# Performance work log

Hardware: AMD Instinct MI355X
Metric: run time of the kernel (lower is better)

## Reference

```python
import jax, jax.numpy as jnp
import numpy as np

B, N, C, DP, H, P = 1, 768, 384, 128, 12, 4
HP3 = H * P * 3


def setup_inputs() -> dict:
    key = jax.random.key(0)
    ks = jax.random.split(key, 16)
    w = lambda k, shp: (jax.random.normal(k, shp, jnp.float32) * 0.02)
    inp = {
        'single': jax.random.normal(ks[0], (B, N, C), jnp.float32),
        'pair': jax.random.normal(ks[1], (B, N, N, DP), jnp.float32),
        'rot': jax.random.normal(ks[2], (B, N, 3, 3), jnp.float32),
        'trans': jax.random.normal(ks[3], (B, N, 3), jnp.float32),
        'q_w': w(ks[4], (C, C)), 'q_b': jnp.zeros((C,), jnp.float32),
        'k_w': w(ks[5], (C, C)), 'k_b': jnp.zeros((C,), jnp.float32),
        'v_w': w(ks[6], (C, C)), 'v_b': jnp.zeros((C,), jnp.float32),
        'pb_w': w(ks[7], (H, DP)), 'pb_b': jnp.zeros((H,), jnp.float32),
        'qp_w': w(ks[8], (HP3, C)), 'qp_b': jnp.zeros((HP3,), jnp.float32),
        'kp_w': w(ks[9], (HP3, C)), 'kp_b': jnp.zeros((HP3,), jnp.float32),
        'vp_w': w(ks[10], (HP3, C)), 'vp_b': jnp.zeros((HP3,), jnp.float32),
        'pt_w': w(ks[11], (C, HP3)), 'pt_b': jnp.zeros((C,), jnp.float32),
        'out_w': w(ks[12], (C, C)), 'out_b': jnp.zeros((C,), jnp.float32),
        'ln_g': jnp.ones((C,), jnp.float32), 'ln_b': jnp.zeros((C,), jnp.float32),
    }
    return inp


def _lin(x, w, b):
    return x @ w.T + b


def reference(single, pair, rot, trans, q_w, q_b, k_w, k_b, v_w, v_b,
              pb_w, pb_b, qp_w, qp_b, kp_w, kp_b, vp_w, vp_b,
              pt_w, pt_b, out_w, out_b, ln_g, ln_b):
    Bs, Ns, Cs = single.shape
    Ch = Cs // H
    scale = Ch ** (-0.5)

    q = _lin(single, q_w, q_b).reshape(Bs, Ns, H, Ch)
    k = _lin(single, k_w, k_b).reshape(Bs, Ns, H, Ch)
    v = _lin(single, v_w, v_b).reshape(Bs, Ns, H, Ch)

    pair_bias = jnp.transpose(_lin(pair, pb_w, pb_b), (0, 3, 1, 2))  # b h i j

    def to_global(w_, b_):
        pts = _lin(single, w_, b_).reshape(Bs, Ns, H, P, 3)
        return jnp.einsum('bnhpi,bnij->bnhpj', pts, rot) + trans[:, :, None, None, :]

    qg = to_global(qp_w, qp_b)
    kg = to_global(kp_w, kp_b)

    q2 = jnp.sum(qg * qg, axis=(3, 4))  # b n h
    k2 = jnp.sum(kg * kg, axis=(3, 4))
    qk = jnp.einsum('bihpd,bjhpd->bijh', qg, kg)
    point_logits = -0.5 * (q2[:, :, None, :] + k2[:, None, :, :] - 2.0 * qk)  # b i j h
    point_logits = jnp.transpose(point_logits, (0, 3, 1, 2)) * scale  # b h i j

    scalar_logits = jnp.einsum('bnhc,bmhc->bhnm', q, k) * scale
    attn = jax.nn.softmax(scalar_logits + pair_bias + point_logits, axis=-1)

    weighted = jnp.einsum('bhnm,bmhc->bnhc', attn, v).reshape(Bs, Ns, Cs)

    vg = to_global(vp_w, vp_b)
    point_weighted = jnp.einsum('bhnm,bmhpd->bnhpd', attn, vg).reshape(Bs, Ns, HP3)
    point_proj = _lin(point_weighted, pt_w, pt_b)

    out = _lin(weighted + point_proj, out_w, out_b)
    x = single + out
    mu = jnp.mean(x, axis=-1, keepdims=True)
    var = jnp.var(x, axis=-1, keepdims=True)
    return (x - mu) / jnp.sqrt(var + 1e-5) * ln_g + ln_b
```

## Files before the change

### kernel.cpp

```cpp
#include <hip/hip_runtime.h>
#include <hip/hip_bf16.h>
#include <cstddef>

#define NN 768
#define CC 384
#define HH 12
#define DPP 128
#define OFF_Q   0
#define OFF_K   294912
#define OFF_V   589824
#define OFF_QP  884736
#define OFF_KP  995328
#define OFF_VP  1105920
#define OFF_WTD 1216512
#define OFF_PW  1511424
#define OFF_LOG 1622016

__global__ __launch_bounds__(256) void k_proj(
    const float* __restrict__ single,
    const float* __restrict__ qw, const float* __restrict__ qb,
    const float* __restrict__ kw, const float* __restrict__ kb,
    const float* __restrict__ vw, const float* __restrict__ vb,
    const float* __restrict__ qpw, const float* __restrict__ qpb,
    const float* __restrict__ kpw, const float* __restrict__ kpb,
    const float* __restrict__ vpw, const float* __restrict__ vpb,
    float* __restrict__ ws)
{
    __shared__ float As[64][33];
    __shared__ float Bs[48][33];
    const int tid = threadIdx.x;
    const int i0 = blockIdx.y * 64;
    const int n0 = blockIdx.x * 48;
    const int tx = tid & 15, ty = tid >> 4;
    float acc[4][3] = {};
    for (int k0 = 0; k0 < CC; k0 += 32) {
        #pragma unroll
        for (int l = tid; l < 64 * 32; l += 256) {
            int r = l >> 5, c = l & 31;
            As[r][c] = single[(size_t)(i0 + r) * CC + k0 + c];
        }
        #pragma unroll
        for (int l = tid; l < 48 * 32; l += 256) {
            int r = l >> 5, c = l & 31;
            int n = n0 + r;
            const float* wp; int row;
            if (n < 1152) { int m = n / CC; row = n - m * CC; wp = (m == 0) ? qw : ((m == 1) ? kw : vw); }
            else { int np = n - 1152; int m = np / 144; row = np - m * 144; wp = (m == 0) ? qpw : ((m == 1) ? kpw : vpw); }
            Bs[r][c] = wp[(size_t)row * CC + k0 + c];
        }
        __syncthreads();
        #pragma unroll
        for (int kk = 0; kk < 32; ++kk) {
            float av[4], bv[3];
            #pragma unroll
            for (int a = 0; a < 4; ++a) av[a] = As[ty * 4 + a][kk];
            #pragma unroll
            for (int b = 0; b < 3; ++b) bv[b] = Bs[tx * 3 + b][kk];
            #pragma unroll
            for (int a = 0; a < 4; ++a)
                #pragma unroll
                for (int b = 0; b < 3; ++b)
                    acc[a][b] = fmaf(av[a], bv[b], acc[a][b]);
        }
        __syncthreads();
    }
    #pragma unroll
    for (int a = 0; a < 4; ++a) {
        int i = i0 + ty * 4 + a;
        #pragma unroll
        for (int b = 0; b < 3; ++b) {
            int n = n0 + tx * 3 + b;
            float bias; size_t dst;
            if (n < 1152) {
                int m = n / CC; int c = n - m * CC;
                bias = ((m == 0) ? qb : ((m == 1) ? kb : vb))[c];
                dst = (size_t)m * 294912 + (size_t)i * CC + c;
            } else {
                int np = n - 1152; int m = np / 144; int c = np - m * 144;
                bias = ((m == 0) ? qpb : ((m == 1) ? kpb : vpb))[c];
                dst = (size_t)OFF_QP + (size_t)m * 110592 + (size_t)i * 144 + c;
            }
            ws[dst] = acc[a][b] + bias;
        }
    }
}

__global__ __launch_bounds__(256) void k_to_global(
    const float* __restrict__ rot, const float* __restrict__ trans, float* __restrict__ ws)
{
    int id = blockIdx.x * 256 + threadIdx.x;
    if (id >= 3 * NN * 48) return;
    int t3 = id / (NN * 48);
    int rem = id - t3 * (NN * 48);
    int n = rem / 48;
    int hp = rem - n * 48;
    float* arr = ws + OFF_QP + (size_t)t3 * 110592 + (size_t)n * 144 + hp * 3;
    float p0 = arr[0], p1 = arr[1], p2 = arr[2];
    const float* R = rot + (size_t)n * 9;
    const float* T = trans + (size_t)n * 3;
    arr[0] = p0 * R[0] + p1 * R[3] + p2 * R[6] + T[0];
    arr[1] = p0 * R[1] + p1 * R[4] + p2 * R[7] + T[1];
    arr[2] = p0 * R[2] + p1 * R[5] + p2 * R[8] + T[2];
}

__global__ __launch_bounds__(256) void k_logits(
    const float* __restrict__ pair,
    const float* __restrict__ pbw, const float* __restrict__ pbb,
    const float* __restrict__ q, const float* __restrict__ k,
    const float* __restrict__ qg, const float* __restrict__ kg,
    float* __restrict__ logits)
{
    const float scale = 0.17677669529663687f;
    __shared__ float pbw_s[HH * DPP];
    const int tid = threadIdx.x;
    for (int idx = tid; idx < HH * DPP; idx += 256) pbw_s[idx] = pbw[idx];
    __syncthreads();
    const int i0 = blockIdx.x * 4;
    const int j = blockIdx.y * 256 + tid;

    float acc[4][12];
    #pragma unroll
    for (int ii = 0; ii < 4; ++ii)
        #pragma unroll
        for (int h = 0; h < HH; ++h) acc[ii][h] = pbb[h];

    #pragma unroll
    for (int ii = 0; ii < 4; ++ii) {
        const float4* pr = (const float4*)(pair + ((size_t)(i0 + ii) * NN + j) * DPP);
        #pragma unroll 4
        for (int k4 = 0; k4 < 32; ++k4) {
            float4 pv = pr[k4];
            #pragma unroll
            for (int h = 0; h < HH; ++h) {
                float4 w = ((const float4*)pbw_s)[h * 32 + k4];
                acc[ii][h] = fmaf(pv.x, w.x, acc[ii][h]);
                acc[ii][h] = fmaf(pv.y, w.y, acc[ii][h]);
                acc[ii][h] = fmaf(pv.z, w.z, acc[ii][h]);
                acc[ii][h] = fmaf(pv.w, w.w, acc[ii][h]);
            }
        }
    }

    #pragma unroll
    for (int h = 0; h < HH; ++h) {
        float kf[32];
        const float4* kp4 = (const float4*)(k + (size_t)j * CC + h * 32);
        #pragma unroll
        for (int t = 0; t < 8; ++t) {
            float4 tv = kp4[t];
            kf[4 * t + 0] = tv.x; kf[4 * t + 1] = tv.y; kf[4 * t + 2] = tv.z; kf[4 * t + 3] = tv.w;
        }
        float kgf[12];
        const float4* kg4 = (const float4*)(kg + (size_t)j * 144 + h * 12);
        #pragma unroll
        for (int t = 0; t < 3; ++t) {
            float4 tv = kg4[t];
            kgf[4 * t + 0] = tv.x; kgf[4 * t + 1] = tv.y; kgf[4 * t + 2] = tv.z; kgf[4 * t + 3] = tv.w;
        }
        #pragma unroll
        for (int ii = 0; ii < 4; ++ii) {
            const float* qrow = q + (size_t)(i0 + ii) * CC + h * 32;
            float dt = 0.f;
            #pragma unroll
            for (int c = 0; c < 32; ++c) dt = fmaf(kf[c], qrow[c], dt);
            const float* qgrow = qg + (size_t)(i0 + ii) * 144 + h * 12;
            float pt = 0.f;
            #pragma unroll
            for (int e = 0; e < 12; ++e) { float d2 = qgrow[e] - kgf[e]; pt = fmaf(d2, d2, pt); }
            float lv = acc[ii][h] + scale * dt - 0.5f * scale * pt;
            logits[((size_t)h * NN + (i0 + ii)) * NN + j] = lv;
        }
    }
}

__global__ __launch_bounds__(256) void k_soft(
    const float* __restrict__ logits, const float* __restrict__ v, const float* __restrict__ vg,
    float* __restrict__ weighted, float* __restrict__ pw)
{
    __shared__ float att[8][772];
    __shared__ float vt[128][45];
    const int tid = threadIdx.x;
    const int h = blockIdx.y;
    const int i0 = blockIdx.x * 8;

    for (int idx = tid; idx < 8 * 192; idx += 256) {
        int r = idx / 192, c4 = idx - r * 192;
        float4 tv = ((const float4*)(logits + ((size_t)h * NN + i0 + r) * NN))[c4];
        float* dp = &att[r][c4 * 4];
        dp[0] = tv.x; dp[1] = tv.y; dp[2] = tv.z; dp[3] = tv.w;
    }
    __syncthreads();
    {
        int r = tid >> 5, lane = tid & 31;
        float m = -1e30f;
        for (int jj = lane; jj < NN; jj += 32) m = fmaxf(m, att[r][jj]);
        #pragma unroll
        for (int off = 16; off; off >>= 1) m = fmaxf(m, __shfl_xor(m, off, 32));
        float s = 0.f;
        for (int jj = lane; jj < NN; jj += 32) { float e = __expf(att[r][jj] - m); att[r][jj] = e; s += e; }
        #pragma unroll
        for (int off = 16; off; off >>= 1) s += __shfl_xor(s, off, 32);
        float inv = 1.f / s;
        for (int jj = lane; jj < NN; jj += 32) att[r][jj] *= inv;
    }
    __syncthreads();

    float acc0 = 0.f, acc1 = 0.f;
    const int o0 = tid, o1 = tid + 256;
    const int r0 = o0 / 44, d0 = o0 - r0 * 44;
    const int o1c = (o1 < 352) ? o1 : 351;
    const int r1 = o1c / 44, d1 = o1c - r1 * 44;
    for (int jc = 0; jc < 6; ++jc) {
        for (int idx = tid; idx < 128 * 44; idx += 256) {
            int jj = idx / 44, d = idx - jj * 44;
            int jg = jc * 128 + jj;
            vt[jj][d] = (d < 32) ? v[(size_t)jg * CC + h * 32 + d]
                                 : vg[(size_t)jg * 144 + h * 12 + (d - 32)];
        }
        __syncthreads();
        const float* a0p = &att[r0][jc * 128];
        const float* a1p = &att[r1][jc * 128];
        #pragma unroll 4
        for (int jj = 0; jj < 128; ++jj) {
            acc0 = fmaf(a0p[jj], vt[jj][d0], acc0);
            acc1 = fmaf(a1p[jj], vt[jj][d1], acc1);
        }
        __syncthreads();
    }
    {
        int i = i0 + r0;
        if (d0 < 32) weighted[(size_t)i * CC + h * 32 + d0] = acc0;
        else         pw[(size_t)i * 144 + h * 12 + (d0 - 32)] = acc0;
    }
    if (o1 < 352) {
        int i = i0 + r1;
        if (d1 < 32) weighted[(size_t)i * CC + h * 32 + d1] = acc1;
        else         pw[(size_t)i * 144 + h * 12 + (d1 - 32)] = acc1;
    }
}

__global__ __launch_bounds__(384) void k_out(
    const float* __restrict__ single,
    const float* __restrict__ weighted, const float* __restrict__ pwv,
    const float* __restrict__ ptw, const float* __restrict__ ptb,
    const float* __restrict__ outw, const float* __restrict__ outb,
    const float* __restrict__ lng, const float* __restrict__ lnb,
    float* __restrict__ out)
{
    __shared__ float pw_s[4][144];
    __shared__ float tmp_s[4][388];
    __shared__ float red[16];
    const int tid = threadIdx.x;
    const int i0 = blockIdx.x * 4;
    for (int idx = tid; idx < 4 * 144; idx += 384) {
        int r = idx / 144, e = idx - r * 144;
        pw_s[r][e] = pwv[(size_t)(i0 + r) * 144 + e];
    }
    __syncthreads();
    const int c = tid;
    float t[4];
    {
        float a[4] = {0.f, 0.f, 0.f, 0.f};
        const float4* wp4 = (const float4*)(ptw + (size_t)c * 144);
        #pragma unroll 4
        for (int e4 = 0; e4 < 36; ++e4) {
            float4 w4 = wp4[e4];
            #pragma unroll
            for (int r = 0; r < 4; ++r) {
                float4 pv = *(const float4*)&pw_s[r][e4 * 4];
                a[r] = fmaf(w4.x, pv.x, a[r]);
                a[r] = fmaf(w4.y, pv.y, a[r]);
                a[r] = fmaf(w4.z, pv.z, a[r]);
                a[r] = fmaf(w4.w, pv.w, a[r]);
            }
        }
        float pb = ptb[c];
        #pragma unroll
        for (int r = 0; r < 4; ++r)
            t[r] = weighted[(size_t)(i0 + r) * CC + c] + pb + a[r];
    }
    #pragma unroll
    for (int r = 0; r < 4; ++r) tmp_s[r][c] = t[r];
    __syncthreads();
    float o[4];
    {
        float ob = outb[c];
        #pragma unroll
        for (int r = 0; r < 4; ++r) o[r] = ob;
        const float4* wp4 = (const float4*)(outw + (size_t)c * CC);
        #pragma unroll 2
        for (int e4 = 0; e4 < 96; ++e4) {
            float4 w4 = wp4[e4];
            #pragma unroll
            for (int r = 0; r < 4; ++r) {
                float4 tv = *(const float4*)&tmp_s[r][e4 * 4];
                o[r] = fmaf(w4.x, tv.x, o[r]);
                o[r] = fmaf(w4.y, tv.y, o[r]);
                o[r] = fmaf(w4.z, tv.z, o[r]);
                o[r] = fmaf(w4.w, tv.w, o[r]);
            }
        }
        #pragma unroll
        for (int r = 0; r < 4; ++r) o[r] += single[(size_t)(i0 + r) * CC + c];
    }
    float g = lng[c], bb = lnb[c];
    #pragma unroll
    for (int rr = 0; rr < 4; ++rr) {
        float xs = o[rr], xq = o[rr] * o[rr];
        #pragma unroll
        for (int off = 32; off; off >>= 1) {
            xs += __shfl_xor(xs, off, 64);
            xq += __shfl_xor(xq, off, 64);
        }
        __syncthreads();
        if ((tid & 63) == 0) { int w = tid >> 6; red[w] = xs; red[8 + w] = xq; }
        __syncthreads();
        float S = red[0] + red[1] + red[2] + red[3] + red[4] + red[5];
        float Q = red[8] + red[9] + red[10] + red[11] + red[12] + red[13];
        float mu = S * (1.f / 384.f);
        float var = Q * (1.f / 384.f) - mu * mu;
        float rs = rsqrtf(var + 1e-5f);
        out[(size_t)(i0 + rr) * CC + c] = (o[rr] - mu) * rs * g + bb;
    }
}

extern "C" void kernel_launch(void* const* d_in, const int* in_sizes, int n_in,
                              void* d_out, int out_size, void* d_ws, size_t ws_size,
                              hipStream_t stream)
{
    const float* single = (const float*)d_in[0];
    const float* pair   = (const float*)d_in[1];
    const float* rot    = (const float*)d_in[2];
    const float* trans  = (const float*)d_in[3];
    const float* qw  = (const float*)d_in[4];  const float* qb  = (const float*)d_in[5];
    const float* kw  = (const float*)d_in[6];  const float* kb  = (const float*)d_in[7];
    const float* vw  = (const float*)d_in[8];  const float* vb  = (const float*)d_in[9];
    const float* pbw = (const float*)d_in[10]; const float* pbb = (const float*)d_in[11];
    const float* qpw = (const float*)d_in[12]; const float* qpb = (const float*)d_in[13];
    const float* kpw = (const float*)d_in[14]; const float* kpb = (const float*)d_in[15];
    const float* vpw = (const float*)d_in[16]; const float* vpb = (const float*)d_in[17];
    const float* ptw = (const float*)d_in[18]; const float* ptb = (const float*)d_in[19];
    const float* outw = (const float*)d_in[20]; const float* outb = (const float*)d_in[21];
    const float* lng  = (const float*)d_in[22]; const float* lnb  = (const float*)d_in[23];

    float* ws = (float*)d_ws;
    float* q   = ws + OFF_Q;
    float* k   = ws + OFF_K;
    float* v   = ws + OFF_V;
    float* qg  = ws + OFF_QP;
    float* kg  = ws + OFF_KP;
    float* vg  = ws + OFF_VP;
    float* wtd = ws + OFF_WTD;
    float* pwv = ws + OFF_PW;
    float* logits = ws + OFF_LOG;

    dim3 g1(33, 12);
    hipLaunchKernelGGL(k_proj, g1, dim3(256), 0, stream,
                       single, qw, qb, kw, kb, vw, vb, qpw, qpb, kpw, kpb, vpw, vpb, ws);
    hipLaunchKernelGGL(k_to_global, dim3(432), dim3(256), 0, stream, rot, trans, ws);
    dim3 g3(192, 3);
    hipLaunchKernelGGL(k_logits, g3, dim3(256), 0, stream,
                       pair, pbw, pbb, q, k, qg, kg, logits);
    dim3 g4(96, 12);
    hipLaunchKernelGGL(k_soft, g4, dim3(256), 0, stream, logits, v, vg, wtd, pwv);
    hipLaunchKernelGGL(k_out, dim3(192), dim3(384), 0, stream,
                       single, wtd, pwv, ptw, ptb, outw, outb, lng, lnb, (float*)d_out);
}
```

Before: 320.7 us.

## Stage pair tiles through LDS with coalesced nontemporal prefetch in logits kernel

```diff
diff --git a/kernel.cpp b/kernel.cpp
--- a/kernel.cpp
+++ b/kernel.cpp
@@ -16,6 +16,8 @@
 #define OFF_PW  1511424
 #define OFF_LOG 1622016
 
+typedef float f32x4 __attribute__((ext_vector_type(4)));
+
 __global__ __launch_bounds__(256) void k_proj(
     const float* __restrict__ single,
     const float* __restrict__ qw, const float* __restrict__ qb,
@@ -103,7 +105,7 @@
     arr[2] = p0 * R[2] + p1 * R[5] + p2 * R[8] + T[2];
 }
 
-__global__ __launch_bounds__(256) void k_logits(
+__global__ __launch_bounds__(256) void k_logits_f(
     const float* __restrict__ pair,
     const float* __restrict__ pbw, const float* __restrict__ pbb,
     const float* __restrict__ q, const float* __restrict__ k,
@@ -111,54 +113,88 @@
     float* __restrict__ logits)
 {
     const float scale = 0.17677669529663687f;
-    __shared__ float pbw_s[HH * DPP];
+    __shared__ float sp[256][33];
     const int tid = threadIdx.x;
-    for (int idx = tid; idx < HH * DPP; idx += 256) pbw_s[idx] = pbw[idx];
-    __syncthreads();
-    const int i0 = blockIdx.x * 4;
-    const int j = blockIdx.y * 256 + tid;
-
-    float acc[4][12];
-    #pragma unroll
-    for (int ii = 0; ii < 4; ++ii)
+    const int i0 = blockIdx.x * 2;
+    const int j0 = blockIdx.y * 256;
+    const int j  = j0 + tid;
+    const float4* w4 = (const float4*)pbw;
+
+    float acc[2][12];
+    #pragma unroll
+    for (int ii = 0; ii < 2; ++ii)
         #pragma unroll
         for (int h = 0; h < HH; ++h) acc[ii][h] = pbb[h];
 
-    #pragma unroll
-    for (int ii = 0; ii < 4; ++ii) {
-        const float4* pr = (const float4*)(pair + ((size_t)(i0 + ii) * NN + j) * DPP);
-        #pragma unroll 4
-        for (int k4 = 0; k4 < 32; ++k4) {
-            float4 pv = pr[k4];
+    const int lrow = tid >> 3;
+    const int lcol = tid & 7;
+
+    f32x4 st[8];
+    {
+        const float* pb0 = pair + ((size_t)i0 * NN + j0) * DPP;
+        #pragma unroll
+        for (int p = 0; p < 8; ++p)
+            st[p] = __builtin_nontemporal_load(
+                (const f32x4*)(pb0 + (size_t)(p * 32 + lrow) * DPP + lcol * 4));
+    }
+    #pragma unroll
+    for (int ph = 0; ph < 8; ++ph) {
+        const int ii = ph >> 2, cc = ph & 3;
+        #pragma unroll
+        for (int p = 0; p < 8; ++p)
+            *(f32x4*)&sp[p * 32 + lrow][lcol * 4] = st[p];
+        __syncthreads();
+        if (ph < 7) {
+            const int iin = (ph + 1) >> 2, ccn = (ph + 1) & 3;
+            const float* pb = pair + ((size_t)(i0 + iin) * NN + j0) * DPP + ccn * 32;
+            #pragma unroll
+            for (int p = 0; p < 8; ++p)
+                st[p] = __builtin_nontemporal_load(
+                    (const f32x4*)(pb + (size_t)(p * 32 + lrow) * DPP + lcol * 4));
+        }
+        #pragma unroll
+        for (int c4 = 0; c4 < 8; ++c4) {
+            float4 pv = *(const float4*)&sp[tid][c4 * 4];
             #pragma unroll
             for (int h = 0; h < HH; ++h) {
-                float4 w = ((const float4*)pbw_s)[h * 32 + k4];
+                float4 w = w4[h * 32 + cc * 8 + c4];
                 acc[ii][h] = fmaf(pv.x, w.x, acc[ii][h]);
                 acc[ii][h] = fmaf(pv.y, w.y, acc[ii][h]);
                 acc[ii][h] = fmaf(pv.z, w.z, acc[ii][h]);
                 acc[ii][h] = fmaf(pv.w, w.w, acc[ii][h]);
             }
         }
+        __syncthreads();
     }
 
     #pragma unroll
     for (int h = 0; h < HH; ++h) {
+        #pragma unroll
+        for (int p = 0; p < 8; ++p) {
+            int row = p * 32 + lrow;
+            *(float4*)&sp[row][lcol * 4] =
+                *(const float4*)(k + (size_t)(j0 + row) * CC + h * 32 + lcol * 4);
+        }
+        __syncthreads();
         float kf[32];
-        const float4* kp4 = (const float4*)(k + (size_t)j * CC + h * 32);
         #pragma unroll
         for (int t = 0; t < 8; ++t) {
-            float4 tv = kp4[t];
-            kf[4 * t + 0] = tv.x; kf[4 * t + 1] = tv.y; kf[4 * t + 2] = tv.z; kf[4 * t + 3] = tv.w;
+            float4 tv = *(const float4*)&sp[tid][t * 4];
+            kf[4 * t + 0] = tv.x; kf[4 * t + 1] = tv.y;
+            kf[4 * t + 2] = tv.z; kf[4 * t + 3] = tv.w;
         }
         float kgf[12];
-        const float4* kg4 = (const float4*)(kg + (size_t)j * 144 + h * 12);
-        #pragma unroll
-        for (int t = 0; t < 3; ++t) {
-            float4 tv = kg4[t];
-            kgf[4 * t + 0] = tv.x; kgf[4 * t + 1] = tv.y; kgf[4 * t + 2] = tv.z; kgf[4 * t + 3] = tv.w;
-        }
-        #pragma unroll
-        for (int ii = 0; ii < 4; ++ii) {
+        {
+            const float4* kg4 = (const float4*)(kg + (size_t)j * 144 + h * 12);
+            #pragma unroll
+            for (int t = 0; t < 3; ++t) {
+                float4 tv = kg4[t];
+                kgf[4 * t + 0] = tv.x; kgf[4 * t + 1] = tv.y;
+                kgf[4 * t + 2] = tv.z; kgf[4 * t + 3] = tv.w;
+            }
+        }
+        #pragma unroll
+        for (int ii = 0; ii < 2; ++ii) {
             const float* qrow = q + (size_t)(i0 + ii) * CC + h * 32;
             float dt = 0.f;
             #pragma unroll
@@ -167,10 +203,16 @@
             float pt = 0.f;
             #pragma unroll
             for (int e = 0; e < 12; ++e) { float d2 = qgrow[e] - kgf[e]; pt = fmaf(d2, d2, pt); }
-            float lv = acc[ii][h] + scale * dt - 0.5f * scale * pt;
-            logits[((size_t)h * NN + (i0 + ii)) * NN + j] = lv;
-        }
-    }
+            acc[ii][h] += scale * dt - 0.5f * scale * pt;
+        }
+        __syncthreads();
+    }
+
+    #pragma unroll
+    for (int ii = 0; ii < 2; ++ii)
+        #pragma unroll
+        for (int h = 0; h < HH; ++h)
+            logits[((size_t)h * NN + (i0 + ii)) * NN + j] = acc[ii][h];
 }
 
 __global__ __launch_bounds__(256) void k_soft(
@@ -185,7 +227,8 @@
 
     for (int idx = tid; idx < 8 * 192; idx += 256) {
         int r = idx / 192, c4 = idx - r * 192;
-        float4 tv = ((const float4*)(logits + ((size_t)h * NN + i0 + r) * NN))[c4];
+        f32x4 tv = __builtin_nontemporal_load(
+            ((const f32x4*)(logits + ((size_t)h * NN + i0 + r) * NN)) + c4);
         float* dp = &att[r][c4 * 4];
         dp[0] = tv.x; dp[1] = tv.y; dp[2] = tv.z; dp[3] = tv.w;
     }
@@ -358,8 +401,8 @@
     hipLaunchKernelGGL(k_proj, g1, dim3(256), 0, stream,
                        single, qw, qb, kw, kb, vw, vb, qpw, qpb, kpw, kpb, vpw, vpb, ws);
     hipLaunchKernelGGL(k_to_global, dim3(432), dim3(256), 0, stream, rot, trans, ws);
-    dim3 g3(192, 3);
-    hipLaunchKernelGGL(k_logits, g3, dim3(256), 0, stream,
+    dim3 g3(384, 3);
+    hipLaunchKernelGGL(k_logits_f, g3, dim3(256), 0, stream,
                        pair, pbw, pbb, q, k, qg, kg, logits);
     dim3 g4(96, 12);
     hipLaunchKernelGGL(k_soft, g4, dim3(256), 0, stream, logits, v, vg, wtd, pwv);
```

After: 581.9 us. +81.4%, slower.

## Split logits reduction across two thread halves with LDS combine

Applied to the files above, without the earlier changes.

```diff
diff --git a/kernel.cpp b/kernel.cpp
--- a/kernel.cpp
+++ b/kernel.cpp
@@ -103,7 +103,7 @@
     arr[2] = p0 * R[2] + p1 * R[5] + p2 * R[8] + T[2];
 }
 
-__global__ __launch_bounds__(256) void k_logits(
+__global__ __launch_bounds__(512) void k_logits2(
     const float* __restrict__ pair,
     const float* __restrict__ pbw, const float* __restrict__ pbb,
     const float* __restrict__ q, const float* __restrict__ k,
@@ -111,28 +111,29 @@
     float* __restrict__ logits)
 {
     const float scale = 0.17677669529663687f;
-    __shared__ float pbw_s[HH * DPP];
+    __shared__ float part[256][13];
     const int tid = threadIdx.x;
-    for (int idx = tid; idx < HH * DPP; idx += 256) pbw_s[idx] = pbw[idx];
-    __syncthreads();
+    const int half = tid >> 8;
+    const int jt = tid & 255;
     const int i0 = blockIdx.x * 4;
-    const int j = blockIdx.y * 256 + tid;
+    const int j = blockIdx.y * 256 + jt;
+    const float4* w4 = (const float4*)pbw;
 
     float acc[4][12];
     #pragma unroll
     for (int ii = 0; ii < 4; ++ii)
         #pragma unroll
-        for (int h = 0; h < HH; ++h) acc[ii][h] = pbb[h];
+        for (int h = 0; h < HH; ++h) acc[ii][h] = (half == 0) ? pbb[h] : 0.f;
 
     #pragma unroll
     for (int ii = 0; ii < 4; ++ii) {
-        const float4* pr = (const float4*)(pair + ((size_t)(i0 + ii) * NN + j) * DPP);
+        const float4* pr = (const float4*)(pair + ((size_t)(i0 + ii) * NN + j) * DPP + half * 64);
         #pragma unroll 4
-        for (int k4 = 0; k4 < 32; ++k4) {
+        for (int k4 = 0; k4 < 16; ++k4) {
             float4 pv = pr[k4];
             #pragma unroll
             for (int h = 0; h < HH; ++h) {
-                float4 w = ((const float4*)pbw_s)[h * 32 + k4];
+                float4 w = w4[h * 32 + half * 16 + k4];
                 acc[ii][h] = fmaf(pv.x, w.x, acc[ii][h]);
                 acc[ii][h] = fmaf(pv.y, w.y, acc[ii][h]);
                 acc[ii][h] = fmaf(pv.z, w.z, acc[ii][h]);
@@ -141,35 +142,60 @@
         }
     }
 
-    #pragma unroll
-    for (int h = 0; h < HH; ++h) {
-        float kf[32];
-        const float4* kp4 = (const float4*)(k + (size_t)j * CC + h * 32);
-        #pragma unroll
-        for (int t = 0; t < 8; ++t) {
-            float4 tv = kp4[t];
-            kf[4 * t + 0] = tv.x; kf[4 * t + 1] = tv.y; kf[4 * t + 2] = tv.z; kf[4 * t + 3] = tv.w;
-        }
-        float kgf[12];
-        const float4* kg4 = (const float4*)(kg + (size_t)j * 144 + h * 12);
-        #pragma unroll
-        for (int t = 0; t < 3; ++t) {
-            float4 tv = kg4[t];
-            kgf[4 * t + 0] = tv.x; kgf[4 * t + 1] = tv.y; kgf[4 * t + 2] = tv.z; kgf[4 * t + 3] = tv.w;
-        }
-        #pragma unroll
-        for (int ii = 0; ii < 4; ++ii) {
-            const float* qrow = q + (size_t)(i0 + ii) * CC + h * 32;
-            float dt = 0.f;
-            #pragma unroll
-            for (int c = 0; c < 32; ++c) dt = fmaf(kf[c], qrow[c], dt);
-            const float* qgrow = qg + (size_t)(i0 + ii) * 144 + h * 12;
-            float pt = 0.f;
-            #pragma unroll
-            for (int e = 0; e < 12; ++e) { float d2 = qgrow[e] - kgf[e]; pt = fmaf(d2, d2, pt); }
-            float lv = acc[ii][h] + scale * dt - 0.5f * scale * pt;
-            logits[((size_t)h * NN + (i0 + ii)) * NN + j] = lv;
-        }
+    {
+        const float4* kp4 = (const float4*)(k + (size_t)j * CC);
+        const float4* kg4 = (const float4*)(kg + (size_t)j * 144);
+        #pragma unroll
+        for (int h = 0; h < HH; ++h) {
+            float kf[16];
+            #pragma unroll
+            for (int t = 0; t < 4; ++t) {
+                float4 tv = kp4[h * 8 + half * 4 + t];
+                kf[4 * t + 0] = tv.x; kf[4 * t + 1] = tv.y;
+                kf[4 * t + 2] = tv.z; kf[4 * t + 3] = tv.w;
+            }
+            float kgf[8];
+            if (half == 0) {
+                float4 a = kg4[h * 3 + 0], b = kg4[h * 3 + 1];
+                kgf[0] = a.x; kgf[1] = a.y; kgf[2] = a.z; kgf[3] = a.w;
+                kgf[4] = b.x; kgf[5] = b.y; kgf[6] = b.z; kgf[7] = b.w;
+            } else {
+                float4 a = kg4[h * 3 + 2];
+                kgf[0] = a.x; kgf[1] = a.y; kgf[2] = a.z; kgf[3] = a.w;
+            }
+            #pragma unroll
+            for (int ii = 0; ii < 4; ++ii) {
+                const float* qrow = q + (size_t)(i0 + ii) * CC + h * 32 + half * 16;
+                float dt = 0.f;
+                #pragma unroll
+                for (int c = 0; c < 16; ++c) dt = fmaf(kf[c], qrow[c], dt);
+                const float* qgrow = qg + (size_t)(i0 + ii) * 144 + h * 12 + half * 8;
+                float pt = 0.f;
+                if (half == 0) {
+                    #pragma unroll
+                    for (int e = 0; e < 8; ++e) { float d2 = qgrow[e] - kgf[e]; pt = fmaf(d2, d2, pt); }
+                } else {
+                    #pragma unroll
+                    for (int e = 0; e < 4; ++e) { float d2 = qgrow[e] - kgf[e]; pt = fmaf(d2, d2, pt); }
+                }
+                acc[ii][h] += scale * dt - 0.5f * scale * pt;
+            }
+        }
+    }
+
+    #pragma unroll
+    for (int ii = 0; ii < 4; ++ii) {
+        if (half == 1) {
+            #pragma unroll
+            for (int h = 0; h < HH; ++h) part[jt][h] = acc[ii][h];
+        }
+        __syncthreads();
+        if (half == 0) {
+            #pragma unroll
+            for (int h = 0; h < HH; ++h)
+                logits[((size_t)h * NN + (i0 + ii)) * NN + j] = acc[ii][h] + part[jt][h];
+        }
+        __syncthreads();
     }
 }
 
@@ -359,7 +385,7 @@
                        single, qw, qb, kw, kb, vw, vb, qpw, qpb, kpw, kpb, vpw, vpb, ws);
     hipLaunchKernelGGL(k_to_global, dim3(432), dim3(256), 0, stream, rot, trans, ws);
     dim3 g3(192, 3);
-    hipLaunchKernelGGL(k_logits, g3, dim3(256), 0, stream,
+    hipLaunchKernelGGL(k_logits2, g3, dim3(512), 0, stream,
                        pair, pbw, pbb, q, k, qg, kg, logits);
     dim3 g4(96, 12);
     hipLaunchKernelGGL(k_soft, g4, dim3(256), 0, stream, logits, v, vg, wtd, pwv);
```

Result: slower. 1.067 ms (+232.8%).
